# Performance work log

Measured on AMD Instinct MI355X. Metric: run time of the kernel, lower is better.

## Reference

```python
import jax, jax.numpy as jnp
import numpy as np

B = 16384  # batch size
DN = ('NCHW', 'OIHW', 'NCHW')


def maxpool2(x):
    # 2x2 max pool, stride 2, VALID (matches nn.MaxPool2d(2, 2))
    return jax.lax.reduce_window(x, -jnp.inf, jax.lax.max,
                                 (1, 1, 2, 2), (1, 1, 2, 2), 'VALID')


def setup_inputs() -> dict:
    key = jax.random.key(0)
    ks = jax.random.split(key, 7)
    return {
        'x': jax.random.normal(ks[0], (B, 1, 32, 32), jnp.float32),
        'w1': jax.random.normal(ks[1], (6, 1, 5, 5), jnp.float32) * 0.1,
        'w2': jax.random.normal(ks[2], (16, 6, 5, 5), jnp.float32) * 0.1,
        'fw1': jax.random.normal(ks[3], (120, 400), jnp.float32) * 0.05,
        'fw2': jax.random.normal(ks[4], (84, 120), jnp.float32) * 0.05,
        'fc3_w': jax.random.normal(ks[5], (10, 84), jnp.float32) * 0.1,
        'fc3_b': jax.random.normal(ks[6], (10,), jnp.float32) * 0.1,
    }


def reference(x, w1, w2, fw1, fw2, fc3_w, fc3_b):
    # conv1 (no bias in StdConv2D) -> relu -> pool
    h = jax.lax.conv_general_dilated(x, w1, (1, 1), 'VALID', dimension_numbers=DN)
    h = maxpool2(jax.nn.relu(h))                      # [B,6,14,14]
    # conv2 -> relu -> pool
    h = jax.lax.conv_general_dilated(h, w2, (1, 1), 'VALID', dimension_numbers=DN)
    h = maxpool2(jax.nn.relu(h))                      # [B,16,5,5]
    h = h.reshape(h.shape[0], 400)                    # channel-major flatten, as torch view
    # StdFC layers: x @ W.T, no bias
    h = jax.nn.relu(h @ fw1.T)                        # [B,120]
    h = jax.nn.relu(h @ fw2.T)                        # [B,84]
    logits = h @ fc3_w.T + fc3_b                      # nn.Linear fc3 with bias
    return jax.nn.softmax(logits, axis=1)
```

## Files before the change

### kernel.cpp

```cpp
#include <hip/hip_runtime.h>
#include <hip/hip_fp16.h>
#include <math.h>

#define TH 512

typedef __attribute__((ext_vector_type(8))) _Float16 half8;
typedef __attribute__((ext_vector_type(4))) float floatx4;

#define P1_S   0
#define X_S    9424
#define P2_S   9424
#define BT_S   18144
#define H1_S   18144
#define H2_S   19232
#define LOG_F  10032
#define W1_U   10416
#define LDS_F  10566

static __device__ __forceinline__ __half2 uash2(unsigned u) {
    union { unsigned u; __half2 h; } v; v.u = u; return v.h;
}
static __device__ __forceinline__ half8 load_h8(const float* row, int kb, int K) {
    int b0 = (kb + 4 <= K) ? kb : (K - 8);
    int b1 = (kb + 8 <= K) ? (kb + 4) : (K - 8);
    float4 w0 = *(const float4*)(row + b0);
    float4 w1 = *(const float4*)(row + b1);
    union { unsigned u[4]; half8 v; } r;
    union { __fp16 __attribute__((ext_vector_type(2))) h; unsigned u; } c;
    c.h = __builtin_amdgcn_cvt_pkrtz(w0.x, w0.y); r.u[0] = c.u;
    c.h = __builtin_amdgcn_cvt_pkrtz(w0.z, w0.w); r.u[1] = c.u;
    c.h = __builtin_amdgcn_cvt_pkrtz(w1.x, w1.y); r.u[2] = c.u;
    c.h = __builtin_amdgcn_cvt_pkrtz(w1.z, w1.w); r.u[3] = c.u;
    return r.v;
}

__global__ __launch_bounds__(TH) void lenet_kernel(
    const float* __restrict__ x,
    const float* __restrict__ w1,
    const float* __restrict__ w2g,
    const float* __restrict__ fw1,
    const float* __restrict__ fw2,
    const float* __restrict__ fc3w,
    const float* __restrict__ fc3b,
    float* __restrict__ out)
{
    __shared__ __align__(16) float sf[LDS_F];
    short* sh = (short*)sf;
    __half* hp = (__half*)sf;
    unsigned* su = (unsigned*)sf;
    const int* p1i = (const int*)sf;

    const int tid  = threadIdx.x;
    const int blk  = blockIdx.x;
    const int lane = tid & 63;
    const int wid  = tid >> 6;
    const int g    = lane >> 4;
    const int cn   = lane & 15;
    const int pr   = cn & 7;
    const int dyr  = cn >> 3;

    {
        float4 xreg[4];
        const float4* xg = (const float4*)(x + (size_t)blk * 8 * 1024);
        #pragma unroll
        for (int j = 0; j < 4; ++j) xreg[j] = xg[tid + j * TH];

        for (int e = tid; e < 150; e += TH)
            ((__half2*)(su + W1_U))[e] = __half2half2(__float2half(w1[e]));
        for (int e = tid; e < 2560; e += TH) {
            int oc = e / 160, kk = e - oc * 160;
            int s = kk >> 5, r = kk & 31;
            float v = 0.f;
            if (r < 30) v = w2g[oc * 150 + (r % 6) * 25 + s * 5 + (r / 6)];
            hp[BT_S + oc * 168 + kk] = __float2half(v);
        }
        #pragma unroll
        for (int j = 0; j < 4; ++j) {
            int e = tid + j * TH;
            int m = e >> 8, rem = e & 255;
            int y = rem >> 3, k4 = rem & 7;
            int off = X_S + m * 1090 + y * 34 + k4 * 4;
            float4 v = xreg[j];
            *(__half2*)(sh + off)     = __floats2half2_rn(v.x, v.y);
            *(__half2*)(sh + off + 2) = __floats2half2_rn(v.z, v.w);
        }
    }
    __syncthreads();

    for (int t = tid; t < 1344; t += TH) {
        int m = t / 168, r = t - m * 168;
        int c = r % 6, q = r / 6;
        int i = q >> 1, hf = q & 1;
        const __half2* wb = (const __half2*)(su + W1_U) + c * 25;
        const int xbase = X_S + m * 1090 + hf * 14;

        __half2 acc0[7], acc1[7];
        #pragma unroll
        for (int j = 0; j < 7; ++j) { acc0[j] = uash2(0u); acc1[j] = uash2(0u); }
        __half2 wprev[5];
        #pragma unroll
        for (int tt = 0; tt < 6; ++tt) {
            unsigned u[9];
            const unsigned* rp = (const unsigned*)(sh + xbase + (2 * i + tt) * 34);
            #pragma unroll
            for (int qq = 0; qq < 9; ++qq) u[qq] = rp[qq];
            __half2 p0[9], p1[8];
            #pragma unroll
            for (int qq = 0; qq < 9; ++qq) p0[qq] = uash2(u[qq]);
            #pragma unroll
            for (int qq = 0; qq < 8; ++qq)
                p1[qq] = uash2(__builtin_amdgcn_perm(u[qq + 1], u[qq], 0x05040302u));

            if (tt < 5) {
                __half2 wc[5];
                #pragma unroll
                for (int kx = 0; kx < 5; ++kx) wc[kx] = wb[tt * 5 + kx];
                #pragma unroll
                for (int j = 0; j < 7; ++j) {
                    acc0[j] = __hfma2(p0[j],     wc[0], acc0[j]);
                    acc0[j] = __hfma2(p1[j],     wc[1], acc0[j]);
                    acc0[j] = __hfma2(p0[j + 1], wc[2], acc0[j]);
                    acc0[j] = __hfma2(p1[j + 1], wc[3], acc0[j]);
                    acc0[j] = __hfma2(p0[j + 2], wc[4], acc0[j]);
                }
                if (tt >= 1) {
                    #pragma unroll
                    for (int j = 0; j < 7; ++j) {
                        acc1[j] = __hfma2(p0[j],     wprev[0], acc1[j]);
                        acc1[j] = __hfma2(p1[j],     wprev[1], acc1[j]);
                        acc1[j] = __hfma2(p0[j + 1], wprev[2], acc1[j]);
                        acc1[j] = __hfma2(p1[j + 1], wprev[3], acc1[j]);
                        acc1[j] = __hfma2(p0[j + 2], wprev[4], acc1[j]);
                    }
                }
                #pragma unroll
                for (int kx = 0; kx < 5; ++kx) wprev[kx] = wc[kx];
            } else {
                #pragma unroll
                for (int j = 0; j < 7; ++j) {
                    acc1[j] = __hfma2(p0[j],     wprev[0], acc1[j]);
                    acc1[j] = __hfma2(p1[j],     wprev[1], acc1[j]);
                    acc1[j] = __hfma2(p0[j + 1], wprev[2], acc1[j]);
                    acc1[j] = __hfma2(p1[j + 1], wprev[3], acc1[j]);
                    acc1[j] = __hfma2(p0[j + 2], wprev[4], acc1[j]);
                }
            }
        }
        __half* dst = hp + P1_S + m * 1178 + i * 84 + hf * 42 + c;
        #pragma unroll
        for (int j = 0; j < 7; ++j) {
            float a0l = __half2float(__low2half(acc0[j]));
            float a0h = __half2float(__high2half(acc0[j]));
            float a1l = __half2float(__low2half(acc1[j]));
            float a1h = __half2float(__high2half(acc1[j]));
            float v = fmaxf(fmaxf(fmaxf(a0l, a0h), fmaxf(a1l, a1h)), 0.f);
            dst[j * 6] = __float2half(v);
        }
    }
    __syncthreads();

    {
        half8 Breg[5];
        #pragma unroll
        for (int s = 0; s < 5; ++s)
            Breg[s] = *(const half8*)(sh + BT_S + cn * 168 + s * 32 + 8 * g);

        if (tid < 192) {
            int im = tid / 24;
            sh[P2_S + im * 424 + 400 + (tid - im * 24)] = 0;
        }

        for (int w = wid; w < 25; w += 8) {
            int i = w / 5, jx = w - 5 * i;
            floatx4 a0 = {0.f,0.f,0.f,0.f}, a1 = {0.f,0.f,0.f,0.f};
            #pragma unroll
            for (int s = 0; s < 5; ++s) {
                #pragma unroll
                for (int dxp = 0; dxp < 2; ++dxp) {
                    int as = pr * 1178 + (2 * i + dyr + s) * 84 + (2 * jx + dxp) * 6 + 8 * g;
                    int ai = as >> 1;
                    union { int4 i4; half8 h8; } a;
                    a.i4.x = p1i[ai];     a.i4.y = p1i[ai + 1];
                    a.i4.z = p1i[ai + 2]; a.i4.w = p1i[ai + 3];
                    floatx4* acc = dxp == 0 ? &a0 : &a1;
                    *acc = __builtin_amdgcn_mfma_f32_16x16x32_f16(a.h8, Breg[s], *acc, 0, 0, 0);
                }
            }
            #pragma unroll
            for (int rg = 0; rg < 4; ++rg) {
                float v = fmaxf(a0[rg], a1[rg]);
                v = fmaxf(v, __shfl_xor(v, 32));
                if (g < 2) {
                    int im = 4 * g + rg;
                    hp[P2_S + im * 424 + cn * 25 + i * 5 + jx] = __float2half(fmaxf(v, 0.f));
                }
            }
        }
    }
    __syncthreads();

    {
        if (tid < 128)
            sh[H1_S + (tid >> 4) * 136 + 120 + (tid & 15)] = 0;
        if (tid >= 128 && tid < 288) {
            int e = tid - 128, im = e / 20;
            sh[H2_S + im * 104 + 84 + (e - im * 20)] = 0;
        }
        int nt = wid;
        floatx4 acc = {0.f,0.f,0.f,0.f};
        int n = nt * 16 + cn;
        const float* wrow = fw1 + (size_t)(n < 120 ? n : 119) * 400;
        for (int ks = 0; ks < 13; ++ks) {
            int kb = ks * 32 + 8 * g;
            half8 b = load_h8(wrow, kb, 400);
            half8 a = *(const half8*)(sh + P2_S + pr * 424 + kb);
            acc = __builtin_amdgcn_mfma_f32_16x16x32_f16(a, b, acc, 0, 0, 0);
        }
        if (g < 2 && n < 120) {
            #pragma unroll
            for (int rg = 0; rg < 4; ++rg)
                hp[H1_S + (4 * g + rg) * 136 + n] = __float2half(fmaxf(acc[rg], 0.f));
        }
    }
    __syncthreads();

    if (wid < 6) {
        floatx4 acc = {0.f,0.f,0.f,0.f};
        int n = wid * 16 + cn;
        const float* wrow = fw2 + (size_t)(n < 84 ? n : 83) * 120;
        for (int ks = 0; ks < 4; ++ks) {
            int kb = ks * 32 + 8 * g;
            half8 b = load_h8(wrow, kb, 120);
            half8 a = *(const half8*)(sh + H1_S + pr * 136 + kb);
            acc = __builtin_amdgcn_mfma_f32_16x16x32_f16(a, b, acc, 0, 0, 0);
        }
        if (g < 2 && n < 84) {
            #pragma unroll
            for (int rg = 0; rg < 4; ++rg)
                hp[H2_S + (4 * g + rg) * 104 + n] = __float2half(fmaxf(acc[rg], 0.f));
        }
    }
    __syncthreads();

    if (wid == 0) {
        floatx4 acc = {0.f,0.f,0.f,0.f};
        int n = cn;
        const float* wrow = fc3w + (size_t)(n < 10 ? n : 9) * 84;
        for (int ks = 0; ks < 3; ++ks) {
            int kb = ks * 32 + 8 * g;
            half8 b = load_h8(wrow, kb, 84);
            half8 a = *(const half8*)(sh + H2_S + pr * 104 + kb);
            acc = __builtin_amdgcn_mfma_f32_16x16x32_f16(a, b, acc, 0, 0, 0);
        }
        if (g < 2 && n < 10) {
            float bias = fc3b[n];
            #pragma unroll
            for (int rg = 0; rg < 4; ++rg)
                sf[LOG_F + (4 * g + rg) * 12 + n] = acc[rg] + bias;
        }
    }
    __syncthreads();

    if (tid < 8) {
        const float* lg = sf + LOG_F + tid * 12;
        float mx = lg[0];
        #pragma unroll
        for (int n = 1; n < 10; ++n) mx = fmaxf(mx, lg[n]);
        float e[10]; float sum = 0.f;
        #pragma unroll
        for (int n = 0; n < 10; ++n) { e[n] = expf(lg[n] - mx); sum += e[n]; }
        float inv = 1.f / sum;
        float* op = out + ((size_t)blk * 8 + tid) * 10;
        #pragma unroll
        for (int n = 0; n < 10; ++n) op[n] = e[n] * inv;
    }
}

extern "C" void kernel_launch(void* const* d_in, const int* in_sizes, int n_in,
                              void* d_out, int out_size, void* d_ws, size_t ws_size,
                              hipStream_t stream) {
    const float* x    = (const float*)d_in[0];
    const float* w1   = (const float*)d_in[1];
    const float* w2   = (const float*)d_in[2];
    const float* fw1  = (const float*)d_in[3];
    const float* fw2  = (const float*)d_in[4];
    const float* fc3w = (const float*)d_in[5];
    const float* fc3b = (const float*)d_in[6];
    float* outp = (float*)d_out;

    dim3 grid(16384 / 8), block(TH);
    hipLaunchKernelGGL(lenet_kernel, grid, block, 0, stream,
                       x, w1, w2, fw1, fw2, fc3w, fc3b, outp);
}
```

Baseline: 89.25 us.

## Move conv1 onto MFMA with interleaved input layout and 256-thread blocks

Replaces the packed-half2 FMA conv1 with MFMA 16x16x32 f16 matrix ops. Input rows are stored pair-interleaved so that each A fragment covers two output rows, and conv1 weights are prebuilt as six banded B matrices. The block size drops from 512 to 256 threads, so each wave now loops over more tiles in the conv2 and FC stages. The aim is to shift conv1 compute from the vector ALUs to the matrix cores. In exchange, many MFMA lanes do padding work, and the narrower block may lower per-block parallelism.

```diff
diff --git a/kernel.cpp b/kernel.cpp
--- a/kernel.cpp
+++ b/kernel.cpp
@@ -2,24 +2,21 @@
 #include <hip/hip_fp16.h>
 #include <math.h>
 
-#define TH 512
+#define TH 256
 
 typedef __attribute__((ext_vector_type(8))) _Float16 half8;
 typedef __attribute__((ext_vector_type(4))) float floatx4;
 
 #define P1_S   0
-#define X_S    9424
+#define XI_S   9424
 #define P2_S   9424
-#define BT_S   18144
-#define H1_S   18144
-#define H2_S   19232
-#define LOG_F  10032
-#define W1_U   10416
-#define LDS_F  10566
-
-static __device__ __forceinline__ __half2 uash2(unsigned u) {
-    union { unsigned u; __half2 h; } v; v.u = u; return v.h;
-}
+#define BT1_S  17936
+#define H1_S   17936
+#define H2_S   19024
+#define LOG_F  9928
+#define BT2_S  21008
+#define LDS_F  11848
+
 static __device__ __forceinline__ half8 load_h8(const float* row, int kb, int K) {
     int b0 = (kb + 4 <= K) ? kb : (K - 8);
     int b1 = (kb + 8 <= K) ? (kb + 4) : (K - 8);
@@ -33,10 +30,16 @@
     c.h = __builtin_amdgcn_cvt_pkrtz(w1.z, w1.w); r.u[3] = c.u;
     return r.v;
 }
+static __device__ __forceinline__ half8 lda(const int* p, int hidx) {
+    int w = hidx >> 1;
+    union { int4 i4; half8 h8; } a;
+    a.i4.x = p[w]; a.i4.y = p[w + 1]; a.i4.z = p[w + 2]; a.i4.w = p[w + 3];
+    return a.h8;
+}
 
 __global__ __launch_bounds__(TH) void lenet_kernel(
     const float* __restrict__ x,
-    const float* __restrict__ w1,
+    const float* __restrict__ w1g,
     const float* __restrict__ w2g,
     const float* __restrict__ fw1,
     const float* __restrict__ fw2,
@@ -47,7 +50,6 @@
     __shared__ __align__(16) float sf[LDS_F];
     short* sh = (short*)sf;
     __half* hp = (__half*)sf;
-    unsigned* su = (unsigned*)sf;
     const int* p1i = (const int*)sf;
 
     const int tid  = threadIdx.x;
@@ -60,101 +62,80 @@
     const int dyr  = cn >> 3;
 
     {
-        float4 xreg[4];
+        float4 xreg[8];
         const float4* xg = (const float4*)(x + (size_t)blk * 8 * 1024);
         #pragma unroll
-        for (int j = 0; j < 4; ++j) xreg[j] = xg[tid + j * TH];
-
-        for (int e = tid; e < 150; e += TH)
-            ((__half2*)(su + W1_U))[e] = __half2half2(__float2half(w1[e]));
+        for (int j = 0; j < 8; ++j) xreg[j] = xg[tid + j * TH];
+
+        for (int e = tid; e < 3072; e += TH) {
+            int b = e >> 9, r = e & 511;
+            int oc = r >> 5, k = r & 31;
+            int xoff = k >> 1, par = k & 1;
+            int row = (int)(((par ? 0x531042u : 0x420531u) >> (4 * b)) & 15u) - 1;
+            float v = 0.f;
+            if (oc < 6 && xoff < 5 && row >= 0) v = w1g[oc * 25 + row * 5 + xoff];
+            hp[BT1_S + e] = __float2half(v);
+        }
         for (int e = tid; e < 2560; e += TH) {
             int oc = e / 160, kk = e - oc * 160;
             int s = kk >> 5, r = kk & 31;
             float v = 0.f;
             if (r < 30) v = w2g[oc * 150 + (r % 6) * 25 + s * 5 + (r / 6)];
-            hp[BT_S + oc * 168 + kk] = __float2half(v);
-        }
-        #pragma unroll
-        for (int j = 0; j < 4; ++j) {
+            hp[BT2_S + oc * 168 + kk] = __float2half(v);
+        }
+        #pragma unroll
+        for (int j = 0; j < 8; ++j) {
             int e = tid + j * TH;
             int m = e >> 8, rem = e & 255;
-            int y = rem >> 3, k4 = rem & 7;
-            int off = X_S + m * 1090 + y * 34 + k4 * 4;
+            int y = rem >> 3, x0 = (rem & 7) * 4;
+            int base = XI_S + m * 1056 + (y >> 1) * 66 + (y & 1);
             float4 v = xreg[j];
-            *(__half2*)(sh + off)     = __floats2half2_rn(v.x, v.y);
-            *(__half2*)(sh + off + 2) = __floats2half2_rn(v.z, v.w);
-        }
-    }
-    __syncthreads();
-
-    for (int t = tid; t < 1344; t += TH) {
-        int m = t / 168, r = t - m * 168;
-        int c = r % 6, q = r / 6;
-        int i = q >> 1, hf = q & 1;
-        const __half2* wb = (const __half2*)(su + W1_U) + c * 25;
-        const int xbase = X_S + m * 1090 + hf * 14;
-
-        __half2 acc0[7], acc1[7];
-        #pragma unroll
-        for (int j = 0; j < 7; ++j) { acc0[j] = uash2(0u); acc1[j] = uash2(0u); }
-        __half2 wprev[5];
-        #pragma unroll
-        for (int tt = 0; tt < 6; ++tt) {
-            unsigned u[9];
-            const unsigned* rp = (const unsigned*)(sh + xbase + (2 * i + tt) * 34);
-            #pragma unroll
-            for (int qq = 0; qq < 9; ++qq) u[qq] = rp[qq];
-            __half2 p0[9], p1[8];
-            #pragma unroll
-            for (int qq = 0; qq < 9; ++qq) p0[qq] = uash2(u[qq]);
-            #pragma unroll
-            for (int qq = 0; qq < 8; ++qq)
-                p1[qq] = uash2(__builtin_amdgcn_perm(u[qq + 1], u[qq], 0x05040302u));
-
-            if (tt < 5) {
-                __half2 wc[5];
+            hp[base + (x0 + 0) * 2] = __float2half(v.x);
+            hp[base + (x0 + 1) * 2] = __float2half(v.y);
+            hp[base + (x0 + 2) * 2] = __float2half(v.z);
+            hp[base + (x0 + 3) * 2] = __float2half(v.w);
+        }
+    }
+    __syncthreads();
+
+    {
+        half8 Bw[6];
+        #pragma unroll
+        for (int b = 0; b < 6; ++b)
+            Bw[b] = *(const half8*)(sh + BT1_S + b * 512 + cn * 32 + 8 * g);
+
+        for (int mi = 0; mi < 2; ++mi) {
+            int m = wid * 2 + mi;
+            for (int cg = 0; cg < 2; ++cg) {
+                int abase = XI_S + m * 1056 + cg * 32 + cn * 2 + 8 * g;
+                half8 fr[3];
+                fr[0] = lda(p1i, abase);
+                fr[1] = lda(p1i, abase + 66);
+                fr[2] = lda(p1i, abase + 132);
                 #pragma unroll
-                for (int kx = 0; kx < 5; ++kx) wc[kx] = wb[tt * 5 + kx];
-                #pragma unroll
-                for (int j = 0; j < 7; ++j) {
-                    acc0[j] = __hfma2(p0[j],     wc[0], acc0[j]);
-                    acc0[j] = __hfma2(p1[j],     wc[1], acc0[j]);
-                    acc0[j] = __hfma2(p0[j + 1], wc[2], acc0[j]);
-                    acc0[j] = __hfma2(p1[j + 1], wc[3], acc0[j]);
-                    acc0[j] = __hfma2(p0[j + 2], wc[4], acc0[j]);
-                }
-                if (tt >= 1) {
-                    #pragma unroll
-                    for (int j = 0; j < 7; ++j) {
-                        acc1[j] = __hfma2(p0[j],     wprev[0], acc1[j]);
-                        acc1[j] = __hfma2(p1[j],     wprev[1], acc1[j]);
-                        acc1[j] = __hfma2(p0[j + 1], wprev[2], acc1[j]);
-                        acc1[j] = __hfma2(p1[j + 1], wprev[3], acc1[j]);
-                        acc1[j] = __hfma2(p0[j + 2], wprev[4], acc1[j]);
+                for (int i = 0; i < 14; ++i) {
+                    half8 fa = fr[i % 3], fb = fr[(i + 1) % 3], fc = fr[(i + 2) % 3];
+                    floatx4 aw0 = {0.f,0.f,0.f,0.f}, aw1 = {0.f,0.f,0.f,0.f};
+                    aw0 = __builtin_amdgcn_mfma_f32_16x16x32_f16(fa, Bw[0], aw0, 0, 0, 0);
+                    aw0 = __builtin_amdgcn_mfma_f32_16x16x32_f16(fb, Bw[1], aw0, 0, 0, 0);
+                    aw0 = __builtin_amdgcn_mfma_f32_16x16x32_f16(fc, Bw[2], aw0, 0, 0, 0);
+                    aw1 = __builtin_amdgcn_mfma_f32_16x16x32_f16(fa, Bw[3], aw1, 0, 0, 0);
+                    aw1 = __builtin_amdgcn_mfma_f32_16x16x32_f16(fb, Bw[4], aw1, 0, 0, 0);
+                    aw1 = __builtin_amdgcn_mfma_f32_16x16x32_f16(fc, Bw[5], aw1, 0, 0, 0);
+                    if (i < 13) fr[i % 3] = lda(p1i, abase + (i + 3) * 66);
+                    if (cn < 6) {
+                        int j0 = cg * 8 + 2 * g;
+                        if (j0 < 14) {
+                            float va = fmaxf(fmaxf(aw0[0], aw0[1]), fmaxf(aw1[0], aw1[1]));
+                            hp[P1_S + m * 1178 + i * 84 + j0 * 6 + cn] =
+                                __float2half(fmaxf(va, 0.f));
+                            float vb = fmaxf(fmaxf(aw0[2], aw0[3]), fmaxf(aw1[2], aw1[3]));
+                            hp[P1_S + m * 1178 + i * 84 + (j0 + 1) * 6 + cn] =
+                                __float2half(fmaxf(vb, 0.f));
+                        }
                     }
                 }
-                #pragma unroll
-                for (int kx = 0; kx < 5; ++kx) wprev[kx] = wc[kx];
-            } else {
-                #pragma unroll
-                for (int j = 0; j < 7; ++j) {
-                    acc1[j] = __hfma2(p0[j],     wprev[0], acc1[j]);
-                    acc1[j] = __hfma2(p1[j],     wprev[1], acc1[j]);
-                    acc1[j] = __hfma2(p0[j + 1], wprev[2], acc1[j]);
-                    acc1[j] = __hfma2(p1[j + 1], wprev[3], acc1[j]);
-                    acc1[j] = __hfma2(p0[j + 2], wprev[4], acc1[j]);
-                }
-            }
-        }
-        __half* dst = hp + P1_S + m * 1178 + i * 84 + hf * 42 + c;
-        #pragma unroll
-        for (int j = 0; j < 7; ++j) {
-            float a0l = __half2float(__low2half(acc0[j]));
-            float a0h = __half2float(__high2half(acc0[j]));
-            float a1l = __half2float(__low2half(acc1[j]));
-            float a1h = __half2float(__high2half(acc1[j]));
-            float v = fmaxf(fmaxf(fmaxf(a0l, a0h), fmaxf(a1l, a1h)), 0.f);
-            dst[j * 6] = __float2half(v);
+            }
         }
     }
     __syncthreads();
@@ -163,14 +144,14 @@
         half8 Breg[5];
         #pragma unroll
         for (int s = 0; s < 5; ++s)
-            Breg[s] = *(const half8*)(sh + BT_S + cn * 168 + s * 32 + 8 * g);
+            Breg[s] = *(const half8*)(sh + BT2_S + cn * 168 + s * 32 + 8 * g);
 
         if (tid < 192) {
             int im = tid / 24;
             sh[P2_S + im * 424 + 400 + (tid - im * 24)] = 0;
         }
 
-        for (int w = wid; w < 25; w += 8) {
+        for (int w = wid; w < 25; w += 4) {
             int i = w / 5, jx = w - 5 * i;
             floatx4 a0 = {0.f,0.f,0.f,0.f}, a1 = {0.f,0.f,0.f,0.f};
             #pragma unroll
@@ -178,12 +159,9 @@
                 #pragma unroll
                 for (int dxp = 0; dxp < 2; ++dxp) {
                     int as = pr * 1178 + (2 * i + dyr + s) * 84 + (2 * jx + dxp) * 6 + 8 * g;
-                    int ai = as >> 1;
-                    union { int4 i4; half8 h8; } a;
-                    a.i4.x = p1i[ai];     a.i4.y = p1i[ai + 1];
-                    a.i4.z = p1i[ai + 2]; a.i4.w = p1i[ai + 3];
+                    half8 a = lda(p1i, as);
                     floatx4* acc = dxp == 0 ? &a0 : &a1;
-                    *acc = __builtin_amdgcn_mfma_f32_16x16x32_f16(a.h8, Breg[s], *acc, 0, 0, 0);
+                    *acc = __builtin_amdgcn_mfma_f32_16x16x32_f16(a, Breg[s], *acc, 0, 0, 0);
                 }
             }
             #pragma unroll
@@ -202,31 +180,32 @@
     {
         if (tid < 128)
             sh[H1_S + (tid >> 4) * 136 + 120 + (tid & 15)] = 0;
-        if (tid >= 128 && tid < 288) {
-            int e = tid - 128, im = e / 20;
+        if (tid >= 96) {
+            int e = tid - 96, im = e / 20;
             sh[H2_S + im * 104 + 84 + (e - im * 20)] = 0;
         }
-        int nt = wid;
+        for (int nt = wid; nt < 8; nt += 4) {
+            floatx4 acc = {0.f,0.f,0.f,0.f};
+            int n = nt * 16 + cn;
+            const float* wrow = fw1 + (size_t)(n < 120 ? n : 119) * 400;
+            for (int ks = 0; ks < 13; ++ks) {
+                int kb = ks * 32 + 8 * g;
+                half8 b = load_h8(wrow, kb, 400);
+                half8 a = *(const half8*)(sh + P2_S + pr * 424 + kb);
+                acc = __builtin_amdgcn_mfma_f32_16x16x32_f16(a, b, acc, 0, 0, 0);
+            }
+            if (g < 2 && n < 120) {
+                #pragma unroll
+                for (int rg = 0; rg < 4; ++rg)
+                    hp[H1_S + (4 * g + rg) * 136 + n] = __float2half(fmaxf(acc[rg], 0.f));
+            }
+        }
+    }
+    __syncthreads();
+
+    for (int nt = wid; nt < 6; nt += 4) {
         floatx4 acc = {0.f,0.f,0.f,0.f};
         int n = nt * 16 + cn;
-        const float* wrow = fw1 + (size_t)(n < 120 ? n : 119) * 400;
-        for (int ks = 0; ks < 13; ++ks) {
-            int kb = ks * 32 + 8 * g;
-            half8 b = load_h8(wrow, kb, 400);
-            half8 a = *(const half8*)(sh + P2_S + pr * 424 + kb);
-            acc = __builtin_amdgcn_mfma_f32_16x16x32_f16(a, b, acc, 0, 0, 0);
-        }
-        if (g < 2 && n < 120) {
-            #pragma unroll
-            for (int rg = 0; rg < 4; ++rg)
-                hp[H1_S + (4 * g + rg) * 136 + n] = __float2half(fmaxf(acc[rg], 0.f));
-        }
-    }
-    __syncthreads();
-
-    if (wid < 6) {
-        floatx4 acc = {0.f,0.f,0.f,0.f};
-        int n = wid * 16 + cn;
         const float* wrow = fw2 + (size_t)(n < 84 ? n : 83) * 120;
         for (int ks = 0; ks < 4; ++ks) {
             int kb = ks * 32 + 8 * g;
```

New measurement: 88.83 us. Within noise of the previous version (-0.5%).
